# Kernel optimization log

Measured on AMD Instinct MI355X. Metric: run time of the kernel, lower is better.

The kernel has to match this reference:

```python
import jax, jax.numpy as jnp
import numpy as np
import math

B, S, D, H = 2, 2048, 1024, 16
DK = D // H


def setup_inputs() -> dict:
    key = jax.random.key(0)
    ks = jax.random.split(key, 8)
    s = 1.0 / math.sqrt(D)
    inp = {
        "query": jax.random.normal(ks[0], (B, S, D), jnp.float32),
        "key": jax.random.normal(ks[1], (B, S, D), jnp.float32),
        "value": jax.random.normal(ks[2], (B, S, D), jnp.float32),
        # causal mask: (1, 1, S, S), 1 where attention allowed
        "mask": jnp.tril(jnp.ones((S, S), jnp.int32))[None, None, :, :],
        "Wq": jax.random.normal(ks[3], (D, D), jnp.float32) * s,
        "Wk": jax.random.normal(ks[4], (D, D), jnp.float32) * s,
        "Wv": jax.random.normal(ks[5], (D, D), jnp.float32) * s,
        "Wo": jax.random.normal(ks[6], (D, D), jnp.float32) * s,
    }
    return inp


def reference(query, key, value, mask, Wq, Wk, Wv, Wo):
    # nn.Linear(bias=False): y = x @ W.T
    def proj_heads(x, W):
        y = jnp.einsum("bsd,ed->bse", x, W)          # (B,S,D)
        return y.reshape(B, -1, H, DK).transpose(0, 2, 1, 3)  # (B,H,S,DK)

    q = proj_heads(query, Wq)
    k = proj_heads(key, Wk)
    v = proj_heads(value, Wv)

    scale = jnp.asarray(math.sqrt(DK), q.dtype)
    scores = jnp.einsum("bhqd,bhkd->bhqk", q, k) / scale  # (B,H,S,S)
    scores = jnp.where(mask == 0, -jnp.inf, scores)
    attn = jax.nn.softmax(scores, axis=-1)
    # dropout p=0.0 (eval): identity
    out = jnp.einsum("bhqk,bhkd->bhqd", attn, v)          # (B,H,S,DK)
    concat = out.transpose(0, 2, 1, 3).reshape(B, -1, D)  # (B,S,D)
    return jnp.einsum("bsd,ed->bse", concat, Wo)
```

## Files before the change

kernel.cpp:

```cpp
#include <hip/hip_runtime.h>
#include <hip/hip_bf16.h>

#define B_ 2
#define S_ 2048
#define D_ 1024
#define H_ 16
#define DK_ 64

typedef __hip_bfloat16 bf16;
typedef __attribute__((ext_vector_type(8))) short bf16x8;
typedef __attribute__((ext_vector_type(4))) short bf16x4;
typedef __attribute__((ext_vector_type(4))) float f32x4;

#define GLDS16(g, l)                                                     \
    __builtin_amdgcn_global_load_lds(                                    \
        (const __attribute__((address_space(1))) void*)(g),              \
        (__attribute__((address_space(3))) void*)(l), 16, 0, 0)

#define MFMA_K32(a, b, c) __builtin_amdgcn_mfma_f32_16x16x32_bf16(a, b, c, 0, 0, 0)
#define MFMA_K16(a, b, c) __builtin_amdgcn_mfma_f32_16x16x16bf16_1k(a, b, c, 0, 0, 0)
#define EXP2F(x) __builtin_amdgcn_exp2f(x)

__global__ __launch_bounds__(256) void cvt_all(
    const float* __restrict__ q, const float* __restrict__ k, const float* __restrict__ v,
    const float* __restrict__ w0, const float* __restrict__ w1,
    const float* __restrict__ w2, const float* __restrict__ w3,
    bf16* __restrict__ oq, bf16* __restrict__ ok, bf16* __restrict__ ov,
    bf16* __restrict__ o0, bf16* __restrict__ o1, bf16* __restrict__ o2,
    bf16* __restrict__ o3) {
    int bid = blockIdx.x;
    const float* src; bf16* dst; int base;
    if      (bid < 2048) { src = q;  dst = oq; base = bid; }
    else if (bid < 4096) { src = k;  dst = ok; base = bid - 2048; }
    else if (bid < 6144) { src = v;  dst = ov; base = bid - 4096; }
    else if (bid < 6656) { src = w0; dst = o0; base = bid - 6144; }
    else if (bid < 7168) { src = w1; dst = o1; base = bid - 6656; }
    else if (bid < 7680) { src = w2; dst = o2; base = bid - 7168; }
    else                 { src = w3; dst = o3; base = bid - 7680; }
    int i = (base * 256 + threadIdx.x) * 8;
    float4 a = *(const float4*)(src + i);
    float4 b = *(const float4*)(src + i + 4);
    __align__(16) bf16 o[8];
    o[0] = __float2bfloat16(a.x); o[1] = __float2bfloat16(a.y);
    o[2] = __float2bfloat16(a.z); o[3] = __float2bfloat16(a.w);
    o[4] = __float2bfloat16(b.x); o[5] = __float2bfloat16(b.y);
    o[6] = __float2bfloat16(b.z); o[7] = __float2bfloat16(b.w);
    *(bf16x8*)(dst + i) = *(const bf16x8*)o;
}

__device__ __forceinline__ void proj_loop32(const bf16* __restrict__ X,
                                            const bf16* __restrict__ W,
                                            int m0, int n0, bf16* As, bf16* Bs,
                                            f32x4 (&acc)[4][4]) {
    const int K = D_;
    const int tid = threadIdx.x;
    const int lane = tid & 63, wave = tid >> 6;
    const int lm = lane & 15, quad = lane >> 4;
    const int wr = wave >> 1, wc = wave & 1;

    auto stage = [&](int t, int bf) {
        int k0 = t * 32;
        bf16* Ab = As + bf * (128 * 32);
        bf16* Bb = Bs + bf * (128 * 32);
#pragma unroll
        for (int i = 0; i < 2; ++i) {
            int s = i * 256 + tid;
            int row = s >> 2, c = (s & 3) ^ (row & 3);
            GLDS16(X + (size_t)(m0 + row) * K + k0 + c * 8, Ab + s * 8);
        }
#pragma unroll
        for (int i = 0; i < 2; ++i) {
            int s = i * 256 + tid;
            int row = s >> 2, c = (s & 3) ^ (row & 3);
            GLDS16(W + (size_t)(n0 + row) * K + k0 + c * 8, Bb + s * 8);
        }
    };

    stage(0, 0);
    for (int t = 0; t < K / 32; ++t) {
        __syncthreads();
        if (t + 1 < K / 32) stage(t + 1, (t + 1) & 1);
        const bf16* Ab = As + (t & 1) * (128 * 32);
        const bf16* Bb = Bs + (t & 1) * (128 * 32);
        bf16x8 aF[4], bF[4];
#pragma unroll
        for (int mt = 0; mt < 4; ++mt) {
            int row = wr * 64 + mt * 16 + lm;
            aF[mt] = *(const bf16x8*)(Ab + row * 32 + ((quad ^ (row & 3)) * 8));
        }
#pragma unroll
        for (int nt = 0; nt < 4; ++nt) {
            int row = wc * 64 + nt * 16 + lm;
            bF[nt] = *(const bf16x8*)(Bb + row * 32 + ((quad ^ (row & 3)) * 8));
        }
#pragma unroll
        for (int mt = 0; mt < 4; ++mt)
#pragma unroll
            for (int nt = 0; nt < 4; ++nt)
                acc[mt][nt] = MFMA_K32(aF[mt], bF[nt], acc[mt][nt]);
    }
}

__global__ __launch_bounds__(256) void proj_qkv(
    const bf16* __restrict__ qx, const bf16* __restrict__ kx, const bf16* __restrict__ vx,
    const bf16* __restrict__ wq, const bf16* __restrict__ wk, const bf16* __restrict__ wv,
    bf16* __restrict__ qb, bf16* __restrict__ kb, bf16* __restrict__ vtb) {
    __shared__ __align__(16) bf16 As[2 * 128 * 32];
    __shared__ __align__(16) bf16 Bs[2 * 128 * 32];
    const int L = (int)blockIdx.x;
    const int tile = (L & 7) * 96 + (L >> 3);
    const int z = tile >> 8;
    const int rem = tile & 255;
    const int n0 = (rem & 7) * 128;
    const int m0 = (rem >> 3) * 128;
    const bf16* X = (z == 0) ? qx : (z == 1) ? kx : vx;
    const bf16* W = (z == 0) ? wq : (z == 1) ? wk : wv;
    f32x4 acc[4][4] = {};
    proj_loop32(X, W, m0, n0, As, Bs, acc);

    const int lane = threadIdx.x & 63, wave = threadIdx.x >> 6;
    const int lm = lane & 15, quad = lane >> 4;
    const int wr = wave >> 1, wc = wave & 1;
#pragma unroll
    for (int mt = 0; mt < 4; ++mt) {
        int mbase = m0 + wr * 64 + mt * 16 + quad * 4;
#pragma unroll
        for (int nt = 0; nt < 4; ++nt) {
            int n = n0 + wc * 64 + nt * 16 + lm;
            if (z == 2) {
                int b = mbase >> 11, s = mbase & (S_ - 1);
                unsigned short u[4];
#pragma unroll
                for (int r = 0; r < 4; ++r) {
                    bf16 hv = __float2bfloat16(acc[mt][nt][r]);
                    u[r] = *(unsigned short*)&hv;
                }
                ushort4 pk = {u[0], u[1], u[2], u[3]};
                *(ushort4*)(vtb + ((size_t)(b * 1024 + n) * S_ + s)) = pk;
            } else {
                bf16* Y = z ? kb : qb;
#pragma unroll
                for (int r = 0; r < 4; ++r)
                    Y[(size_t)(mbase + r) * D_ + n] = __float2bfloat16(acc[mt][nt][r]);
            }
        }
    }
}

__global__ __launch_bounds__(256) void proj_o(const bf16* __restrict__ X,
                                              const bf16* __restrict__ W,
                                              float* __restrict__ Y) {
    __shared__ __align__(16) bf16 As[2 * 64 * 32];
    __shared__ __align__(16) bf16 Bs[2 * 128 * 32];
    const int L = (int)blockIdx.x;
    const int tile = (L & 7) * 64 + (L >> 3);
    const int n0 = (tile & 7) * 128;
    const int m0 = (tile >> 3) * 64;

    const int K = D_;
    const int tid = threadIdx.x;
    const int lane = tid & 63, wave = tid >> 6;
    const int lm = lane & 15, quad = lane >> 4;
    const int wr = wave >> 1, wc = wave & 1;

    f32x4 acc[2][4] = {};

    auto stage = [&](int t, int bf) {
        int k0 = t * 32;
        bf16* Ab = As + bf * (64 * 32);
        bf16* Bb = Bs + bf * (128 * 32);
        {
            int s = tid;
            int row = s >> 2, c = (s & 3) ^ (row & 3);
            GLDS16(X + (size_t)(m0 + row) * K + k0 + c * 8, Ab + s * 8);
        }
#pragma unroll
        for (int i = 0; i < 2; ++i) {
            int s = i * 256 + tid;
            int row = s >> 2, c = (s & 3) ^ (row & 3);
            GLDS16(W + (size_t)(n0 + row) * K + k0 + c * 8, Bb + s * 8);
        }
    };

    stage(0, 0);
    for (int t = 0; t < K / 32; ++t) {
        __syncthreads();
        if (t + 1 < K / 32) stage(t + 1, (t + 1) & 1);
        const bf16* Ab = As + (t & 1) * (64 * 32);
        const bf16* Bb = Bs + (t & 1) * (128 * 32);
        bf16x8 aF[2], bF[4];
#pragma unroll
        for (int mt = 0; mt < 2; ++mt) {
            int row = wr * 32 + mt * 16 + lm;
            aF[mt] = *(const bf16x8*)(Ab + row * 32 + ((quad ^ (row & 3)) * 8));
        }
#pragma unroll
        for (int nt = 0; nt < 4; ++nt) {
            int row = wc * 64 + nt * 16 + lm;
            bF[nt] = *(const bf16x8*)(Bb + row * 32 + ((quad ^ (row & 3)) * 8));
        }
#pragma unroll
        for (int mt = 0; mt < 2; ++mt)
#pragma unroll
            for (int nt = 0; nt < 4; ++nt)
                acc[mt][nt] = MFMA_K32(aF[mt], bF[nt], acc[mt][nt]);
    }

#pragma unroll
    for (int mt = 0; mt < 2; ++mt) {
        int mbase = m0 + wr * 32 + mt * 16 + quad * 4;
#pragma unroll
        for (int nt = 0; nt < 4; ++nt) {
            int n = n0 + wc * 64 + nt * 16 + lm;
#pragma unroll
            for (int r = 0; r < 4; ++r)
                Y[(size_t)(mbase + r) * D_ + n] = acc[mt][nt][r];
        }
    }
}

__global__ __launch_bounds__(512) void attn_kernel(const bf16* __restrict__ Q,
                                                   const bf16* __restrict__ Kb,
                                                   const bf16* __restrict__ VT,
                                                   bf16* __restrict__ O) {
    __shared__ __align__(16) bf16 kt[2][128 * 64];
    __shared__ __align__(16) bf16 vt[2][64 * 128];

    const int tid = threadIdx.x;
    const int lane = tid & 63, wave = tid >> 6;
    const int lm = lane & 15, quad = lane >> 4;
    const int f = (int)blockIdx.x;
    const int cls = f & 7;
    const int t = f >> 3;
    const int qi = (t < 32) ? (15 - (t >> 2)) : ((t >> 2) - 8);
    const int combo = cls + 8 * (t & 3);
    const int b = combo >> 4, h = combo & 15;
    const int q0 = qi * 128 + wave * 16;

    const size_t bhoff = (size_t)b * S_ * D_ + (size_t)h * DK_;
    const bf16* vtb = VT + ((size_t)b * 1024 + h * DK_) * S_;

    const bf16* qp = Q + bhoff + (size_t)(q0 + lm) * D_ + quad * 8;
    bf16x8 aq0 = *(const bf16x8*)(qp);
    bf16x8 aq1 = *(const bf16x8*)(qp + 32);

    f32x4 oacc[4] = {};
    float lsum = 0.f;
    const float cexp = 0.125f * 1.44269504f;

    auto stage = [&](int i, int bf) {
        int j0s = i * 128;
#pragma unroll
        for (int ii = 0; ii < 2; ++ii) {
            int s = ii * 512 + tid;
            int j = s >> 3, c = (s & 7) ^ (j & 7);
            GLDS16(Kb + bhoff + (size_t)(j0s + j) * D_ + c * 8, kt[bf] + s * 8);
        }
#pragma unroll
        for (int ii = 0; ii < 2; ++ii) {
            int s = ii * 512 + tid;
            int d = s >> 4, c = (s & 15) ^ (d & 15);
            GLDS16(vtb + (size_t)d * S_ + j0s + c * 8, vt[bf] + s * 8);
        }
    };

    auto chunk = [&](const bf16* ktb, const bf16* vtl, int st, bool mk) {
        int j = st * 16 + lm;
        bf16x8 bk0 = *(const bf16x8*)(ktb + (((j << 3) | (quad ^ (j & 7))) * 8));
        bf16x8 bk1 = *(const bf16x8*)(ktb + (((j << 3) | ((4 + quad) ^ (j & 7))) * 8));
        f32x4 z = {};
        __builtin_amdgcn_s_setprio(1);
        z = MFMA_K32(bk0, aq0, z);
        z = MFMA_K32(bk1, aq1, z);
        __builtin_amdgcn_s_setprio(0);
        bf16x4 pa;
        float rs = 0.f;
#pragma unroll
        for (int r = 0; r < 4; ++r) {
            float p = EXP2F(z[r] * cexp);
            if (mk && (quad * 4 + r > lm)) p = 0.f;
            rs += p;
            bf16 hv = __float2bfloat16(p);
            pa[r] = *(short*)&hv;
        }
        lsum += rs;
        __builtin_amdgcn_s_setprio(1);
#pragma unroll
        for (int dt = 0; dt < 4; ++dt) {
            int d = dt * 16 + lm;
            int cl = st * 2 + (quad >> 1);
            bf16x4 bv = *(const bf16x4*)(vtl + d * 128 +
                                         ((cl ^ (d & 15)) * 8 + (quad & 1) * 4));
            oacc[dt] = MFMA_K16(pa, bv, oacc[dt]);
        }
        __builtin_amdgcn_s_setprio(0);
    };

    stage(0, 0);

    for (int i = 0; i <= qi; ++i) {
        __syncthreads();
        if (i < qi) stage(i + 1, (i + 1) & 1);
        const bf16* ktb = kt[i & 1];
        const bf16* vtl = vt[i & 1];
        if (i < qi) {
#pragma unroll
            for (int st = 0; st < 8; ++st) chunk(ktb, vtl, st, false);
        } else {
            for (int st = 0; st < wave; ++st) chunk(ktb, vtl, st, false);
            chunk(ktb, vtl, wave, true);
        }
    }

    float l = lsum;
    l += __shfl_xor(l, 16, 64);
    l += __shfl_xor(l, 32, 64);
#pragma unroll
    for (int r = 0; r < 4; ++r) {
        float inv = 1.f / __shfl(l, quad * 4 + r, 64);
        int qrow = q0 + quad * 4 + r;
#pragma unroll
        for (int dt = 0; dt < 4; ++dt) {
            int d = dt * 16 + lm;
            O[bhoff + (size_t)qrow * D_ + d] = __float2bfloat16(oacc[dt][r] * inv);
        }
    }
}

extern "C" void kernel_launch(void* const* d_in, const int* in_sizes, int n_in,
                              void* d_out, int out_size, void* d_ws, size_t ws_size,
                              hipStream_t stream) {
    const float* q_in = (const float*)d_in[0];
    const float* k_in = (const float*)d_in[1];
    const float* v_in = (const float*)d_in[2];
    const float* Wq_f = (const float*)d_in[4];
    const float* Wk_f = (const float*)d_in[5];
    const float* Wv_f = (const float*)d_in[6];
    const float* Wo_f = (const float*)d_in[7];
    float* out = (float*)d_out;

    const size_t NEL = (size_t)B_ * S_ * D_;
    const size_t WEL = (size_t)D_ * D_;
    bf16* p = (bf16*)d_ws;
    bf16* qx = p;  p += NEL;
    bf16* kx = p;  p += NEL;
    bf16* vx = p;  p += NEL;
    bf16* wq = p;  p += WEL;
    bf16* wk = p;  p += WEL;
    bf16* wv = p;  p += WEL;
    bf16* wo = p;  p += WEL;
    bf16* qb = p;  p += NEL;
    bf16* kb = p;  p += NEL;
    bf16* vtb = p; p += NEL;
    bf16* cb = p;  p += NEL;

    cvt_all<<<8192, 256, 0, stream>>>(q_in, k_in, v_in, Wq_f, Wk_f, Wv_f, Wo_f,
                                      qx, kx, vx, wq, wk, wv, wo);

    proj_qkv<<<dim3(768), 256, 0, stream>>>(qx, kx, vx, wq, wk, wv, qb, kb, vtb);

    attn_kernel<<<dim3(512), 512, 0, stream>>>(qb, kb, vtb, cb);

    proj_o<<<dim3(512), 256, 0, stream>>>(cb, wo, out);
}
```

Baseline: 221.6 us.

## Pair complementary causal query tiles per block to balance attention work

```diff
diff --git a/kernel.cpp b/kernel.cpp
--- a/kernel.cpp
+++ b/kernel.cpp
@@ -232,20 +232,25 @@
     const int f = (int)blockIdx.x;
     const int cls = f & 7;
     const int t = f >> 3;
-    const int qi = (t < 32) ? (15 - (t >> 2)) : ((t >> 2) - 8);
+    const int p = t >> 2;
     const int combo = cls + 8 * (t & 3);
     const int b = combo >> 4, h = combo & 15;
-    const int q0 = qi * 128 + wave * 16;
+    const int qiA = p, qiB = 15 - p;
+    const int q0A = qiA * 128 + wave * 16;
+    const int q0B = qiB * 128 + wave * 16;
 
     const size_t bhoff = (size_t)b * S_ * D_ + (size_t)h * DK_;
     const bf16* vtb = VT + ((size_t)b * 1024 + h * DK_) * S_;
 
-    const bf16* qp = Q + bhoff + (size_t)(q0 + lm) * D_ + quad * 8;
-    bf16x8 aq0 = *(const bf16x8*)(qp);
-    bf16x8 aq1 = *(const bf16x8*)(qp + 32);
-
-    f32x4 oacc[4] = {};
-    float lsum = 0.f;
+    const bf16* qpA = Q + bhoff + (size_t)(q0A + lm) * D_ + quad * 8;
+    bf16x8 aqA0 = *(const bf16x8*)(qpA);
+    bf16x8 aqA1 = *(const bf16x8*)(qpA + 32);
+    const bf16* qpB = Q + bhoff + (size_t)(q0B + lm) * D_ + quad * 8;
+    bf16x8 aqB0 = *(const bf16x8*)(qpB);
+    bf16x8 aqB1 = *(const bf16x8*)(qpB + 32);
+
+    f32x4 oaccA[4] = {}, oaccB[4] = {};
+    float lsumA = 0.f, lsumB = 0.f;
     const float cexp = 0.125f * 1.44269504f;
 
     auto stage = [&](int i, int bf) {
@@ -264,27 +269,25 @@
         }
     };
 
-    auto chunk = [&](const bf16* ktb, const bf16* vtl, int st, bool mk) {
+    auto chunk = [&](const bf16* ktb, const bf16* vtl, int st, bool mk,
+                     bf16x8 aq0, bf16x8 aq1, f32x4 (&oacc)[4], float& lsum) {
         int j = st * 16 + lm;
         bf16x8 bk0 = *(const bf16x8*)(ktb + (((j << 3) | (quad ^ (j & 7))) * 8));
         bf16x8 bk1 = *(const bf16x8*)(ktb + (((j << 3) | ((4 + quad) ^ (j & 7))) * 8));
         f32x4 z = {};
-        __builtin_amdgcn_s_setprio(1);
         z = MFMA_K32(bk0, aq0, z);
         z = MFMA_K32(bk1, aq1, z);
-        __builtin_amdgcn_s_setprio(0);
         bf16x4 pa;
         float rs = 0.f;
 #pragma unroll
         for (int r = 0; r < 4; ++r) {
-            float p = EXP2F(z[r] * cexp);
-            if (mk && (quad * 4 + r > lm)) p = 0.f;
-            rs += p;
-            bf16 hv = __float2bfloat16(p);
+            float pv = EXP2F(z[r] * cexp);
+            if (mk && (quad * 4 + r > lm)) pv = 0.f;
+            rs += pv;
+            bf16 hv = __float2bfloat16(pv);
             pa[r] = *(short*)&hv;
         }
         lsum += rs;
-        __builtin_amdgcn_s_setprio(1);
 #pragma unroll
         for (int dt = 0; dt < 4; ++dt) {
             int d = dt * 16 + lm;
@@ -293,38 +296,55 @@
                                          ((cl ^ (d & 15)) * 8 + (quad & 1) * 4));
             oacc[dt] = MFMA_K16(pa, bv, oacc[dt]);
         }
-        __builtin_amdgcn_s_setprio(0);
-    };
-
+    };
+
+    const int nt = qiB + 1;
     stage(0, 0);
 
-    for (int i = 0; i <= qi; ++i) {
+    for (int i = 0; i < nt; ++i) {
         __syncthreads();
-        if (i < qi) stage(i + 1, (i + 1) & 1);
+        if (i + 1 < nt) stage(i + 1, (i + 1) & 1);
         const bf16* ktb = kt[i & 1];
         const bf16* vtl = vt[i & 1];
-        if (i < qi) {
-#pragma unroll
-            for (int st = 0; st < 8; ++st) chunk(ktb, vtl, st, false);
+
+        if (i < qiB) {
+#pragma unroll
+            for (int st = 0; st < 8; ++st)
+                chunk(ktb, vtl, st, false, aqB0, aqB1, oaccB, lsumB);
         } else {
-            for (int st = 0; st < wave; ++st) chunk(ktb, vtl, st, false);
-            chunk(ktb, vtl, wave, true);
-        }
-    }
-
-    float l = lsum;
-    l += __shfl_xor(l, 16, 64);
-    l += __shfl_xor(l, 32, 64);
-#pragma unroll
-    for (int r = 0; r < 4; ++r) {
-        float inv = 1.f / __shfl(l, quad * 4 + r, 64);
-        int qrow = q0 + quad * 4 + r;
-#pragma unroll
-        for (int dt = 0; dt < 4; ++dt) {
-            int d = dt * 16 + lm;
-            O[bhoff + (size_t)qrow * D_ + d] = __float2bfloat16(oacc[dt][r] * inv);
-        }
-    }
+            for (int st = 0; st < wave; ++st)
+                chunk(ktb, vtl, st, false, aqB0, aqB1, oaccB, lsumB);
+            chunk(ktb, vtl, wave, true, aqB0, aqB1, oaccB, lsumB);
+        }
+
+        if (i < qiA) {
+#pragma unroll
+            for (int st = 0; st < 8; ++st)
+                chunk(ktb, vtl, st, false, aqA0, aqA1, oaccA, lsumA);
+        } else if (i == qiA) {
+            for (int st = 0; st < wave; ++st)
+                chunk(ktb, vtl, st, false, aqA0, aqA1, oaccA, lsumA);
+            chunk(ktb, vtl, wave, true, aqA0, aqA1, oaccA, lsumA);
+        }
+    }
+
+    auto finish = [&](float lsum, f32x4 (&oacc)[4], int q0) {
+        float l = lsum;
+        l += __shfl_xor(l, 16, 64);
+        l += __shfl_xor(l, 32, 64);
+#pragma unroll
+        for (int r = 0; r < 4; ++r) {
+            float inv = 1.f / __shfl(l, quad * 4 + r, 64);
+            int qrow = q0 + quad * 4 + r;
+#pragma unroll
+            for (int dt = 0; dt < 4; ++dt) {
+                int d = dt * 16 + lm;
+                O[bhoff + (size_t)qrow * D_ + d] = __float2bfloat16(oacc[dt][r] * inv);
+            }
+        }
+    };
+    finish(lsumA, oaccA, q0A);
+    finish(lsumB, oaccB, q0B);
 }
 
 extern "C" void kernel_launch(void* const* d_in, const int* in_sizes, int n_in,
@@ -359,7 +379,7 @@
 
     proj_qkv<<<dim3(768), 256, 0, stream>>>(qx, kx, vx, wq, wk, wv, qb, kb, vtb);
 
-    attn_kernel<<<dim3(512), 512, 0, stream>>>(qb, kb, vtb, cb);
+    attn_kernel<<<dim3(256), 512, 0, stream>>>(qb, kb, vtb, cb);
 
     proj_o<<<dim3(512), 256, 0, stream>>>(cb, wo, out);
 }
```

Measured after the change: 223.9 us. No clear change (+1.0%).
